# Kernel optimization log

Measured on AMD Instinct MI355X. Metric: run time of the kernel, lower is better.

Reference implementation:

```python
import jax, jax.numpy as jnp
import numpy as np

# Layer geometry (matches init_kwargs): input_dims=[16,32,16] -> F=16 filters, S=32*16=512 shifts; O=32 output filters
F = 16
S = 512
O = 32
B = 256


def setup_inputs() -> dict:
    key = jax.random.key(0)
    k1, k2, k3 = jax.random.split(key, 3)
    x = jax.random.normal(k1, (B, S * F), dtype=jnp.float32)
    W = jax.random.normal(k2, (S * F, O), dtype=jnp.float32)
    b = jax.random.normal(k3, (O,), dtype=jnp.float32)
    return {"x": x, "W": W, "b": b}


def reference(x, W, b):
    # x: [B, S*F] -> [B, S, F]; W: [S*F, O] -> [S, F, O]
    xs = x.reshape(-1, S, F)
    w = W.reshape(S, F, O)
    # Contraction dim of the original tf.matmul is 1, so it is a broadcast
    # multiply producing a [B, S, F, O] intermediate.
    prod = xs[:, :, :, None] * w[None, :, :, :]   # [B, S, F, O]
    pre = jnp.sum(jnp.max(prod, axis=1), axis=1) + b  # max over shifts, sum over filters -> [B, O]
    return jax.nn.relu(pre)
```

## Files before the change

kernel.cpp:

```cpp
#include <hip/hip_runtime.h>

#define FDIM 16
#define SDIM 512
#define ODIM 32
#define SF   (SDIM * FDIM)
#define PAIRS (FDIM * ODIM)
#define NCHUNK 4
#define CH   (SDIM / NCHUNK)

__global__ __launch_bounds__(512) void max_layer_kernel(
    const float* __restrict__ x, const float* __restrict__ W,
    const float* __restrict__ bias, float* __restrict__ out) {
  __shared__ float xs[SF];
  __shared__ float red[NCHUNK * PAIRS];

  const int t = threadIdx.x;
  const int b = blockIdx.x;

  const float4* xin = (const float4*)(x + b * SF);
  float4* xsv = (float4*)xs;
  for (int i = t; i < SF / 4; i += 512) xsv[i] = xin[i];
  __syncthreads();

  const int tq = t & 127;
  const int sc = t >> 7;
  const int f  = tq >> 3;

  const float NEG = -3.402823466e+38f;
  float4 m = make_float4(NEG, NEG, NEG, NEG);

  const float4* wp = (const float4*)W + (size_t)sc * CH * (PAIRS / 4) + tq;
  const float*  xp = xs + sc * CH * FDIM + f;

#pragma unroll 4
  for (int i = 0; i < CH; ++i) {
    float4 w = wp[i * (PAIRS / 4)];
    float xv = xp[i * FDIM];
    m.x = fmaxf(m.x, xv * w.x);
    m.y = fmaxf(m.y, xv * w.y);
    m.z = fmaxf(m.z, xv * w.z);
    m.w = fmaxf(m.w, xv * w.w);
  }

  ((float4*)red)[sc * (PAIRS / 4) + tq] = m;
  __syncthreads();

  float mm = 0.0f;
  if (t < PAIRS) {
    mm = fmaxf(fmaxf(red[t], red[PAIRS + t]),
               fmaxf(red[2 * PAIRS + t], red[3 * PAIRS + t]));
  }
  __syncthreads();
  if (t < PAIRS) red[t] = mm;
  __syncthreads();

  if (t < ODIM) {
    float s = bias[t];
#pragma unroll
    for (int ff = 0; ff < FDIM; ++ff) s += red[ff * ODIM + t];
    out[b * ODIM + t] = fmaxf(s, 0.0f);
  }
}

extern "C" void kernel_launch(void* const* d_in, const int* in_sizes, int n_in,
                              void* d_out, int out_size, void* d_ws, size_t ws_size,
                              hipStream_t stream) {
  const float* x    = (const float*)d_in[0];
  const float* W    = (const float*)d_in[1];
  const float* bias = (const float*)d_in[2];
  float* out        = (float*)d_out;
  max_layer_kernel<<<dim3(256), dim3(512), 0, stream>>>(x, W, bias, out);
}
```

Measured before the change: 71.76 us.

## Tile over batch and shift chunks to reuse W across eight batches, add reduction pass

```diff
diff --git a/kernel.cpp b/kernel.cpp
--- a/kernel.cpp
+++ b/kernel.cpp
@@ -4,56 +4,89 @@
 #define SDIM 512
 #define ODIM 32
 #define SF   (SDIM * FDIM)
-#define PAIRS (FDIM * ODIM)
-#define NCHUNK 4
-#define CH   (SDIM / NCHUNK)
+#define PAIRS 512
+#define NB   8
+#define SC   32
+#define NSC  (SDIM / SC)
+#define NBG  (256 / NB)
 
-__global__ __launch_bounds__(512) void max_layer_kernel(
+__global__ __launch_bounds__(256) void max_layer_phase1(
     const float* __restrict__ x, const float* __restrict__ W,
-    const float* __restrict__ bias, float* __restrict__ out) {
-  __shared__ float xs[SF];
-  __shared__ float red[NCHUNK * PAIRS];
+    float* __restrict__ part) {
+  __shared__ float xs[NB * SC * FDIM];
+  __shared__ float red[NB * PAIRS];
 
-  const int t = threadIdx.x;
-  const int b = blockIdx.x;
+  const int t  = threadIdx.x;
+  const int bg = blockIdx.x / NSC;
+  const int sc = blockIdx.x % NSC;
 
-  const float4* xin = (const float4*)(x + b * SF);
-  float4* xsv = (float4*)xs;
-  for (int i = t; i < SF / 4; i += 512) xsv[i] = xin[i];
+  const float4* xin = (const float4*)x;
+  float4* xs4 = (float4*)xs;
+  for (int i = t; i < NB * SC * FDIM / 4; i += 256) {
+    int b   = i / (SC * FDIM / 4);
+    int off = i % (SC * FDIM / 4);
+    xs4[i] = xin[(size_t)(bg * NB + b) * (SF / 4) + sc * (SC * FDIM / 4) + off];
+  }
   __syncthreads();
 
   const int tq = t & 127;
-  const int sc = t >> 7;
+  const int th = t >> 7;
   const int f  = tq >> 3;
 
   const float NEG = -3.402823466e+38f;
-  float4 m = make_float4(NEG, NEG, NEG, NEG);
+  float4 macc[NB];
+#pragma unroll
+  for (int b = 0; b < NB; ++b) macc[b] = make_float4(NEG, NEG, NEG, NEG);
 
-  const float4* wp = (const float4*)W + (size_t)sc * CH * (PAIRS / 4) + tq;
-  const float*  xp = xs + sc * CH * FDIM + f;
+  const float4* wp = (const float4*)W + (size_t)(sc * SC) * (PAIRS / 4) + tq;
 
 #pragma unroll 4
-  for (int i = 0; i < CH; ++i) {
-    float4 w = wp[i * (PAIRS / 4)];
-    float xv = xp[i * FDIM];
-    m.x = fmaxf(m.x, xv * w.x);
-    m.y = fmaxf(m.y, xv * w.y);
-    m.z = fmaxf(m.z, xv * w.z);
-    m.w = fmaxf(m.w, xv * w.w);
+  for (int j = 0; j < SC / 2; ++j) {
+    const int s = th * (SC / 2) + j;
+    float4 w = wp[s * (PAIRS / 4)];
+    const float* xp = xs + s * FDIM + f;
+#pragma unroll
+    for (int b = 0; b < NB; ++b) {
+      float xv = xp[b * SC * FDIM];
+      macc[b].x = fmaxf(macc[b].x, xv * w.x);
+      macc[b].y = fmaxf(macc[b].y, xv * w.y);
+      macc[b].z = fmaxf(macc[b].z, xv * w.z);
+      macc[b].w = fmaxf(macc[b].w, xv * w.w);
+    }
   }
 
-  ((float4*)red)[sc * (PAIRS / 4) + tq] = m;
-  __syncthreads();
-
-  float mm = 0.0f;
-  if (t < PAIRS) {
-    mm = fmaxf(fmaxf(red[t], red[PAIRS + t]),
-               fmaxf(red[2 * PAIRS + t], red[3 * PAIRS + t]));
+  if (th == 1) {
+#pragma unroll
+    for (int b = 0; b < NB; ++b) ((float4*)red)[b * 128 + tq] = macc[b];
   }
   __syncthreads();
-  if (t < PAIRS) red[t] = mm;
+  if (th == 0) {
+#pragma unroll
+    for (int b = 0; b < NB; ++b) {
+      float4 o = ((float4*)red)[b * 128 + tq];
+      o.x = fmaxf(o.x, macc[b].x);
+      o.y = fmaxf(o.y, macc[b].y);
+      o.z = fmaxf(o.z, macc[b].z);
+      o.w = fmaxf(o.w, macc[b].w);
+      ((float4*)part)[((size_t)(bg * NB + b) * NSC + sc) * (PAIRS / 4) + tq] = o;
+    }
+  }
+}
+
+__global__ __launch_bounds__(256) void max_layer_phase2(
+    const float* __restrict__ part, const float* __restrict__ bias,
+    float* __restrict__ out) {
+  __shared__ float red[PAIRS];
+  const int t = threadIdx.x;
+  const int b = blockIdx.x;
+  const float* pb = part + (size_t)b * NSC * PAIRS;
+  for (int p = t; p < PAIRS; p += 256) {
+    float m = pb[p];
+#pragma unroll
+    for (int c = 1; c < NSC; ++c) m = fmaxf(m, pb[c * PAIRS + p]);
+    red[p] = m;
+  }
   __syncthreads();
-
   if (t < ODIM) {
     float s = bias[t];
 #pragma unroll
@@ -69,5 +102,8 @@
   const float* W    = (const float*)d_in[1];
   const float* bias = (const float*)d_in[2];
   float* out        = (float*)d_out;
-  max_layer_kernel<<<dim3(256), dim3(512), 0, stream>>>(x, W, bias, out);
+  float* part       = (float*)d_ws;
+
+  max_layer_phase1<<<dim3(NBG * NSC), dim3(256), 0, stream>>>(x, W, part);
+  max_layer_phase2<<<dim3(256), dim3(256), 0, stream>>>(part, bias, out);
 }
```

After: 69.44 us. 1.03x faster.
